# Optimization experiments

Measured on AMD Instinct MI355X. Metric: run time of the kernel, lower is better.

## Reference

```python
import jax, jax.numpy as jnp
import numpy as np

NS, NP, EJ, ER = 10000, 2048, 32768, 32768  # skills, job/resume pairs, edges
D, H = 1536, 8
NEG_SLOPE_ATT = 0.2   # GAT attention leaky_relu
NEG_SLOPE = 0.01      # F.leaky_relu / nn.LeakyReLU default


def setup_inputs() -> dict:
    key = jax.random.key(0)
    ks = jax.random.split(key, 20)
    rn = lambda k, shp, s=1.0: jax.random.normal(k, shp, dtype=jnp.float32) * s
    s_d = 1.0 / np.sqrt(D)
    return {
        "x_skill": rn(ks[0], (NS, D)),
        "x_job": rn(ks[1], (NP, D)),
        "x_resume": rn(ks[2], (NP, D)),
        # GraphConv params (lin_rel has bias, lin_root bias=False in PyG)
        "W_rel": rn(ks[3], (D, D), s_d),
        "b_rel": jnp.zeros((D,), jnp.float32),
        "W_root": rn(ks[4], (D, D), s_d),
        # GATConv params (heads=8, concat=False)
        "W_gat_src": rn(ks[5], (D, H * D), s_d),
        "W_gat_dst": rn(ks[6], (D, H * D), s_d),
        "att_src": rn(ks[7], (H, D), s_d),
        "att_dst": rn(ks[8], (H, D), s_d),
        "b_gat": jnp.zeros((D,), jnp.float32),
        # MLP: [3072 -> 512 -> 128 -> 1]
        "W1": rn(ks[9], (2 * D, 512), 1.0 / np.sqrt(2 * D)),
        "b1": jnp.zeros((512,), jnp.float32),
        "W2": rn(ks[10], (512, 128), 1.0 / np.sqrt(512)),
        "b2": jnp.zeros((128,), jnp.float32),
        "W3": rn(ks[11], (128, 1), 1.0 / np.sqrt(128)),
        "b3": jnp.zeros((1,), jnp.float32),
        # edge lists (src = skill idx, dst = job/resume idx)
        "edge_src_job": jax.random.randint(ks[12], (EJ,), 0, NS, dtype=jnp.int32),
        "edge_dst_job": jax.random.randint(ks[13], (EJ,), 0, NP, dtype=jnp.int32),
        "edge_src_res": jax.random.randint(ks[14], (ER,), 0, NS, dtype=jnp.int32),
        "edge_dst_res": jax.random.randint(ks[15], (ER,), 0, NP, dtype=jnp.int32),
    }


def reference(x_skill, x_job, x_resume, W_rel, b_rel, W_root,
              W_gat_src, W_gat_dst, att_src, att_dst, b_gat,
              W1, b1, W2, b2, W3, b3,
              edge_src_job, edge_dst_job, edge_src_res, edge_dst_res):
    n_pair = x_job.shape[0]

    # --- GraphConv (skill -> job): sum-aggregate then linear + root ---
    agg = jax.ops.segment_sum(x_skill[edge_src_job], edge_dst_job,
                              num_segments=n_pair)                  # [NP, D]
    h_job = agg @ W_rel + b_rel + x_job @ W_root                     # [NP, D]

    # --- GATConv (skill -> resume), heads=H, concat=False, no self-loops ---
    xs = (x_skill @ W_gat_src).reshape(-1, H, D)                     # [NS, H, D]
    xd = (x_resume @ W_gat_dst).reshape(-1, H, D)                    # [NP, H, D]
    a_src = jnp.einsum('nhd,hd->nh', xs, att_src)                    # [NS, H]
    a_dst = jnp.einsum('nhd,hd->nh', xd, att_dst)                    # [NP, H]
    e = jax.nn.leaky_relu(a_src[edge_src_res] + a_dst[edge_dst_res],
                          NEG_SLOPE_ATT)                             # [E, H]
    # segment softmax over edges grouped by destination resume node
    e_max = jax.ops.segment_max(e, edge_dst_res, num_segments=n_pair)
    e_exp = jnp.exp(e - e_max[edge_dst_res])
    denom = jax.ops.segment_sum(e_exp, edge_dst_res, num_segments=n_pair)
    alpha = e_exp / (denom[edge_dst_res] + 1e-16)                    # [E, H]
    msg = xs[edge_src_res] * alpha[:, :, None]                       # [E, H, D]
    out = jax.ops.segment_sum(msg, edge_dst_res, num_segments=n_pair)  # [NP, H, D]
    h_res = out.mean(axis=1) + b_gat                                 # concat=False -> head mean

    # --- combine + MLP ---
    h = jnp.concatenate([jax.nn.leaky_relu(h_job, NEG_SLOPE),
                         jax.nn.leaky_relu(h_res, NEG_SLOPE)], axis=1)  # [NP, 2D]
    h = jax.nn.leaky_relu(h @ W1 + b1, NEG_SLOPE)
    h = jax.nn.leaky_relu(h @ W2 + b2, NEG_SLOPE)
    score = (h @ W3 + b3).squeeze(-1)                                # [NP]
    return score, alpha
```

## Files before the change

### kernel.cpp

```cpp
#include <hip/hip_runtime.h>

#define D_ 1536
#define H_ 8

typedef __attribute__((ext_vector_type(8))) short bf16x8;
typedef __attribute__((ext_vector_type(4))) float f32x4;

__device__ __forceinline__ unsigned short f2bf(float f) {
    unsigned u = __builtin_bit_cast(unsigned, f);
    unsigned r = (u + 0x7fffu + ((u >> 16) & 1u)) >> 16;
    return (unsigned short)r;
}

__device__ __forceinline__ unsigned pack2bf(float a, float b) {
    return (unsigned)f2bf(a) | ((unsigned)f2bf(b) << 16);
}

__device__ __forceinline__ float bflo(unsigned u) { return __builtin_bit_cast(float, u << 16); }
__device__ __forceinline__ float bfhi(unsigned u) { return __builtin_bit_cast(float, u & 0xffff0000u); }

__device__ __forceinline__ void gload16(const void* g, void* l) {
    __builtin_amdgcn_global_load_lds((const __attribute__((address_space(1))) void*)g,
                                     (__attribute__((address_space(3))) void*)l, 16, 0, 0);
}

__global__ __launch_bounds__(256) void k_vmat2(const float* __restrict__ Wsrc,
                                               const float* __restrict__ Wdst,
                                               const float* __restrict__ att_s,
                                               const float* __restrict__ att_d,
                                               float* __restrict__ Vsrc,
                                               float* __restrict__ Vdst) {
    int id = blockIdx.x;
    int sel = id >= D_;
    int d = sel ? id - D_ : id;
    const float4* wr = (const float4*)((sel ? Wdst : Wsrc) + (size_t)d * (H_ * D_));
    const float* at = sel ? att_d : att_s;
    int t = threadIdx.x;
    float part[H_];
    #pragma unroll
    for (int h = 0; h < H_; h++) {
        const float4* ar = (const float4*)(at + h * D_);
        float4 w0 = wr[h * 384 + t];
        float4 a0 = ar[t];
        float s = w0.x * a0.x + w0.y * a0.y + w0.z * a0.z + w0.w * a0.w;
        if (t < 128) {
            float4 w1 = wr[h * 384 + 256 + t];
            float4 a1 = ar[256 + t];
            s += w1.x * a1.x + w1.y * a1.y + w1.z * a1.z + w1.w * a1.w;
        }
        part[h] = s;
    }
    __shared__ float red[4][H_];
    int lane = t & 63, w = t >> 6;
    #pragma unroll
    for (int h = 0; h < H_; h++) {
        float v = part[h];
        for (int o = 32; o; o >>= 1) v += __shfl_down(v, o);
        if (lane == 0) red[w][h] = v;
    }
    __syncthreads();
    if (t < H_) (sel ? Vdst : Vsrc)[d * H_ + t] = red[0][t] + red[1][t] + red[2][t] + red[3][t];
}

__global__ __launch_bounds__(256) void k_a_xsb(const float* __restrict__ x,
                                               const float* __restrict__ V,
                                               float* __restrict__ out,
                                               unsigned* __restrict__ xb) {
    int n = blockIdx.x;
    float part[H_] = {};
    const float2* xr = (const float2*)x + (size_t)n * 768;
    unsigned* ob = xb + (size_t)n * 768;
    #pragma unroll
    for (int j = 0; j < 3; j++) {
        int e = threadIdx.x + j * 256;
        float2 v = xr[e];
        ob[e] = pack2bf(v.x, v.y);
        const float* vp = V + (size_t)(2 * e) * H_;
        #pragma unroll
        for (int h = 0; h < H_; h++) part[h] += v.x * vp[h] + v.y * vp[h + H_];
    }
    __shared__ float red[4][H_];
    int lane = threadIdx.x & 63, w = threadIdx.x >> 6;
    #pragma unroll
    for (int h = 0; h < H_; h++) {
        float v = part[h];
        for (int o = 32; o; o >>= 1) v += __shfl_down(v, o);
        if (lane == 0) red[w][h] = v;
    }
    __syncthreads();
    if (threadIdx.x < H_)
        out[(size_t)n * H_ + threadIdx.x] =
            red[0][threadIdx.x] + red[1][threadIdx.x] + red[2][threadIdx.x] + red[3][threadIdx.x];
}

__global__ __launch_bounds__(256) void k_a(const float* __restrict__ x,
                                           const float* __restrict__ V,
                                           float* __restrict__ out, int N) {
    int n = blockIdx.x;
    if (n >= N) return;
    float part[H_] = {};
    const float* xr = x + (size_t)n * D_;
    #pragma unroll
    for (int j = 0; j < 6; j++) {
        int d = threadIdx.x + j * 256;
        float xv = xr[d];
        const float* vp = V + d * H_;
        #pragma unroll
        for (int h = 0; h < H_; h++) part[h] += xv * vp[h];
    }
    __shared__ float red[4][H_];
    int lane = threadIdx.x & 63, w = threadIdx.x >> 6;
    #pragma unroll
    for (int h = 0; h < H_; h++) {
        float v = part[h];
        for (int o = 32; o; o >>= 1) v += __shfl_down(v, o);
        if (lane == 0) red[w][h] = v;
    }
    __syncthreads();
    if (threadIdx.x < H_)
        out[(size_t)n * H_ + threadIdx.x] =
            red[0][threadIdx.x] + red[1][threadIdx.x] + red[2][threadIdx.x] + red[3][threadIdx.x];
}

__global__ void k_count(const int* __restrict__ dj, int ej, const int* __restrict__ dr, int er,
                        int* cnt_j, int* cnt_r) {
    int i = blockIdx.x * blockDim.x + threadIdx.x;
    if (i < ej) atomicAdd(&cnt_j[dj[i]], 1);
    else if (i < ej + er) atomicAdd(&cnt_r[dr[i - ej]], 1);
}

__global__ void k_scan(const int* __restrict__ cnt_j, int* off_j,
                       const int* __restrict__ cnt_r, int* off_r, int NP) {
    const int* cnt = blockIdx.x ? cnt_r : cnt_j;
    int* off = blockIdx.x ? off_r : off_j;
    int lane = threadIdx.x;
    int chunk = (NP + 63) / 64;
    int base = lane * chunk;
    int sum = 0;
    for (int i = 0; i < chunk; i++) { int idx = base + i; if (idx < NP) sum += cnt[idx]; }
    int incl = sum;
    for (int o = 1; o < 64; o <<= 1) { int t = __shfl_up(incl, o); if (lane >= o) incl += t; }
    int run = incl - sum;
    for (int i = 0; i < chunk; i++) { int idx = base + i; if (idx < NP) { off[idx] = run; run += cnt[idx]; } }
    if (lane == 63) off[NP] = run;
}

__global__ void k_scatter(const int* __restrict__ dj, int ej, const int* __restrict__ dr, int er,
                          const int* __restrict__ off_j, int* fill_j, int* sid_j,
                          const int* __restrict__ off_r, int* fill_r, int* sid_r) {
    int i = blockIdx.x * blockDim.x + threadIdx.x;
    if (i < ej) {
        int p = dj[i];
        int slot = atomicAdd(&fill_j[p], 1);
        sid_j[off_j[p] + slot] = i;
    } else if (i < ej + er) {
        int e = i - ej;
        int p = dr[e];
        int slot = atomicAdd(&fill_r[p], 1);
        sid_r[off_r[p] + slot] = e;
    }
}

__global__ __launch_bounds__(256) void k_agg(const unsigned* __restrict__ xb, const int* __restrict__ src,
                                             const int* __restrict__ sid, const int* __restrict__ cnt,
                                             const int* __restrict__ off,
                                             const float* __restrict__ x_job,
                                             unsigned* __restrict__ cat_u) {
    int p = blockIdx.x;
    int n = cnt[p], o = off[p];
    float2 acc[3] = {};
    int i = 0;
    for (; i + 2 <= n; i += 2) {
        int e0 = sid[o + i], e1 = sid[o + i + 1];
        const unsigned* r0 = xb + (size_t)src[e0] * 768 + threadIdx.x;
        const unsigned* r1 = xb + (size_t)src[e1] * 768 + threadIdx.x;
        unsigned v0[3], v1[3];
        #pragma unroll
        for (int j = 0; j < 3; j++) { v0[j] = r0[j * 256]; v1[j] = r1[j * 256]; }
        #pragma unroll
        for (int j = 0; j < 3; j++) {
            acc[j].x += bflo(v0[j]) + bflo(v1[j]);
            acc[j].y += bfhi(v0[j]) + bfhi(v1[j]);
        }
    }
    if (i < n) {
        int e0 = sid[o + i];
        const unsigned* r0 = xb + (size_t)src[e0] * 768 + threadIdx.x;
        #pragma unroll
        for (int j = 0; j < 3; j++) { unsigned v = r0[j * 256]; acc[j].x += bflo(v); acc[j].y += bfhi(v); }
    }
    unsigned* orow = cat_u + (size_t)p * 1536 + threadIdx.x;
    #pragma unroll
    for (int j = 0; j < 3; j++) orow[j * 256] = pack2bf(acc[j].x, acc[j].y);
    const float2* xjr = (const float2*)x_job + (size_t)p * 768 + threadIdx.x;
    #pragma unroll
    for (int j = 0; j < 3; j++) { float2 v = xjr[j * 256]; orow[768 + j * 256] = pack2bf(v.x, v.y); }
}

__global__ void k_softmax(const float* __restrict__ a_src, const float* __restrict__ a_dst,
                          const int* __restrict__ src, const int* __restrict__ sid,
                          const int* __restrict__ cnt, const int* __restrict__ off,
                          float* __restrict__ alpha_out) {
    int p = blockIdx.x;
    int n = cnt[p], o = off[p];
    if (n == 0) return;
    int lane = threadIdx.x;
    #pragma unroll 1
    for (int h = 0; h < H_; h++) {
        float ad = a_dst[(size_t)p * H_ + h];
        float m = -3.4e38f;
        for (int i = lane; i < n; i += 64) {
            int e = sid[o + i];
            float v = a_src[(size_t)src[e] * H_ + h] + ad;
            v = v >= 0.f ? v : 0.2f * v;
            m = fmaxf(m, v);
        }
        for (int o2 = 32; o2; o2 >>= 1) m = fmaxf(m, __shfl_xor(m, o2));
        float s = 0.f;
        for (int i = lane; i < n; i += 64) {
            int e = sid[o + i];
            float v = a_src[(size_t)src[e] * H_ + h] + ad;
            v = v >= 0.f ? v : 0.2f * v;
            s += expf(v - m);
        }
        for (int o2 = 32; o2; o2 >>= 1) s += __shfl_xor(s, o2);
        float inv = 1.f / (s + 1e-16f);
        for (int i = lane; i < n; i += 64) {
            int e = sid[o + i];
            float v = a_src[(size_t)src[e] * H_ + h] + ad;
            v = v >= 0.f ? v : 0.2f * v;
            alpha_out[(size_t)e * H_ + h] = expf(v - m) * inv;
        }
    }
}

__global__ __launch_bounds__(256) void k_aggatt(const unsigned* __restrict__ xb,
                                                const float* __restrict__ alpha,
                                                const int* __restrict__ src, const int* __restrict__ sid,
                                                const int* __restrict__ cnt, const int* __restrict__ off,
                                                unsigned* __restrict__ aggatt_u) {
    int p = blockIdx.x;
    int n = cnt[p], o = off[p];
    float2 acc[H_][3] = {};
    int i = 0;
    for (; i + 2 <= n; i += 2) {
        int e0 = sid[o + i], e1 = sid[o + i + 1];
        const unsigned* r0 = xb + (size_t)src[e0] * 768 + threadIdx.x;
        const unsigned* r1 = xb + (size_t)src[e1] * 768 + threadIdx.x;
        unsigned v0[3], v1[3];
        #pragma unroll
        for (int j = 0; j < 3; j++) { v0[j] = r0[j * 256]; v1[j] = r1[j * 256]; }
        const float* a0 = alpha + (size_t)e0 * H_;
        const float* a1 = alpha + (size_t)e1 * H_;
        float f0[3][2], f1[3][2];
        #pragma unroll
        for (int j = 0; j < 3; j++) {
            f0[j][0] = bflo(v0[j]); f0[j][1] = bfhi(v0[j]);
            f1[j][0] = bflo(v1[j]); f1[j][1] = bfhi(v1[j]);
        }
        #pragma unroll
        for (int h = 0; h < H_; h++) {
            float w0 = a0[h], w1 = a1[h];
            #pragma unroll
            for (int j = 0; j < 3; j++) {
                acc[h][j].x += w0 * f0[j][0] + w1 * f1[j][0];
                acc[h][j].y += w0 * f0[j][1] + w1 * f1[j][1];
            }
        }
    }
    if (i < n) {
        int e0 = sid[o + i];
        const unsigned* r0 = xb + (size_t)src[e0] * 768 + threadIdx.x;
        unsigned v0[3];
        #pragma unroll
        for (int j = 0; j < 3; j++) v0[j] = r0[j * 256];
        const float* a0 = alpha + (size_t)e0 * H_;
        #pragma unroll
        for (int h = 0; h < H_; h++) {
            float w0 = a0[h];
            #pragma unroll
            for (int j = 0; j < 3; j++) {
                acc[h][j].x += w0 * bflo(v0[j]);
                acc[h][j].y += w0 * bfhi(v0[j]);
            }
        }
    }
    unsigned* orow = aggatt_u + (size_t)p * (H_ * 768) + threadIdx.x;
    #pragma unroll
    for (int h = 0; h < H_; h++)
        #pragma unroll
        for (int j = 0; j < 3; j++)
            orow[h * 768 + j * 256] = pack2bf(acc[h][j].x, acc[h][j].y);
}

template <int GATB>
__global__ __launch_bounds__(256) void k_tr(const float* __restrict__ in, int ldin,
                                            unsigned short* __restrict__ out, int ldout) {
    __shared__ float t[64][65];
    int k0 = blockIdx.y * 64, n0 = blockIdx.x * 64;
    int tx = threadIdx.x & 63, ty = threadIdx.x >> 6;
    #pragma unroll
    for (int i = 0; i < 16; i++) {
        int k = k0 + ty + i * 4;
        const float* rp;
        if (GATB) {
            int d2 = k % D_, h = k / D_;
            rp = in + (size_t)d2 * (H_ * D_) + (size_t)h * D_;
        } else {
            rp = in + (size_t)k * ldin;
        }
        t[ty + i * 4][tx] = rp[n0 + tx];
    }
    __syncthreads();
    int tx2 = threadIdx.x & 31, ty2 = threadIdx.x >> 5;
    #pragma unroll
    for (int i = 0; i < 8; i++) {
        int nl = ty2 + i * 8;
        unsigned v = pack2bf(t[tx2 * 2][nl], t[tx2 * 2 + 1][nl]);
        *(unsigned*)(out + (size_t)(n0 + nl) * ldout + k0 + tx2 * 2) = v;
    }
}

__global__ __launch_bounds__(512, 4) void gemm_sk(const unsigned short* __restrict__ A, int lda,
                                                  const unsigned short* __restrict__ BT, int ldb,
                                                  float* __restrict__ P, int N, int bs, int extra) {
    __shared__ unsigned short As[3][256 * 32];
    __shared__ unsigned short Bs[3][128 * 32];
    int tid = threadIdx.x;
    int lane = tid & 63, wid = tid >> 6;

    int nwg = gridDim.x * gridDim.y;
    int bidh = blockIdx.y * gridDim.x + blockIdx.x;
    int swz = (bidh & 7) * (nwg >> 3) + (bidh >> 3);
    int bn = (swz % gridDim.x) * 128;
    int bm = (swz / gridDim.x) * 256;

    int z = blockIdx.z;
    int nt = bs + (z < extra);
    int kb = z * bs + min(z, extra);
    int kbase = kb * 32;

    int wr = wid >> 1, wc = wid & 1;
    int fr = lane & 15, g = lane >> 4;

    int ra0 = tid >> 2, sa0 = tid & 3;
    int ra1 = (tid + 512) >> 2;
    int sg_a0 = sa0 ^ ((ra0 >> 1) & 3);
    int sg_a1 = sa0 ^ ((ra1 >> 1) & 3);
    int sg_b = sg_a0;

    f32x4 acc[4][4] = {};

    auto stage = [&](int buf, int k0) {
        gload16(A + (size_t)(bm + ra0) * lda + k0 + sg_a0 * 8, &As[buf][tid * 8]);
        gload16(A + (size_t)(bm + ra1) * lda + k0 + sg_a1 * 8, &As[buf][(tid + 512) * 8]);
        gload16(BT + (size_t)(bn + ra0) * ldb + k0 + sg_b * 8, &Bs[buf][tid * 8]);
    };

    stage(0, kbase);
    if (nt > 1) stage(1, kbase + 32);
    for (int t = 0; t < nt; t++) {
        if (t + 2 < nt) {
            stage((t + 2) % 3, kbase + (t + 2) * 32);
            asm volatile("s_waitcnt vmcnt(6)" ::: "memory");
        } else if (t + 1 < nt) {
            asm volatile("s_waitcnt vmcnt(3)" ::: "memory");
        } else {
            asm volatile("s_waitcnt vmcnt(0)" ::: "memory");
        }
        __builtin_amdgcn_s_barrier();
        __builtin_amdgcn_sched_barrier(0);
        int cur = t % 3;
        bf16x8 a[4], b[4];
        #pragma unroll
        for (int mi = 0; mi < 4; mi++) {
            int row = wr * 64 + mi * 16 + fr;
            a[mi] = *(const bf16x8*)(&As[cur][row * 32 + ((g ^ ((row >> 1) & 3)) * 8)]);
        }
        #pragma unroll
        for (int ni = 0; ni < 4; ni++) {
            int row = wc * 64 + ni * 16 + fr;
            b[ni] = *(const bf16x8*)(&Bs[cur][row * 32 + ((g ^ ((row >> 1) & 3)) * 8)]);
        }
        __builtin_amdgcn_s_setprio(1);
        #pragma unroll
        for (int mi = 0; mi < 4; mi++)
            #pragma unroll
            for (int ni = 0; ni < 4; ni++)
                acc[mi][ni] = __builtin_amdgcn_mfma_f32_16x16x32_bf16(a[mi], b[ni], acc[mi][ni], 0, 0, 0);
        __builtin_amdgcn_s_setprio(0);
        __builtin_amdgcn_s_barrier();
        __builtin_amdgcn_sched_barrier(0);
    }

    size_t MN = (size_t)N * (size_t)(gridDim.y * 256);
    float* Pz = P + (size_t)z * MN;
    #pragma unroll
    for (int mi = 0; mi < 4; mi++) {
        int r0 = bm + wr * 64 + mi * 16 + (lane >> 4) * 4;
        #pragma unroll
        for (int ni = 0; ni < 4; ni++) {
            int c = bn + wc * 64 + ni * 16 + (lane & 15);
            #pragma unroll
            for (int j = 0; j < 4; j++)
                Pz[(size_t)(r0 + j) * N + c] = acc[mi][ni][j];
        }
    }
}

template <int OUT_BF16>
__global__ __launch_bounds__(256) void k_reduce(const float* __restrict__ P, int S, int MN, int N,
                                                void* __restrict__ Cout, int ldc,
                                                const float* __restrict__ bias, float scale,
                                                int useLeaky) {
    int idx = (blockIdx.x * 256 + threadIdx.x) * 4;
    if (idx >= MN) return;
    float4 v = *(const float4*)(P + idx);
    for (int s = 1; s < S; s++) {
        float4 t = *(const float4*)(P + (size_t)s * MN + idx);
        v.x += t.x; v.y += t.y; v.z += t.z; v.w += t.w;
    }
    int m = idx / N, n = idx - m * N;
    float vv[4] = {v.x, v.y, v.z, v.w};
    #pragma unroll
    for (int j = 0; j < 4; j++) {
        float x = vv[j] * scale + bias[n + j];
        if (useLeaky) x = x >= 0.f ? x : 0.01f * x;
        if (OUT_BF16) ((unsigned short*)Cout)[(size_t)m * ldc + n + j] = f2bf(x);
        else ((float*)Cout)[(size_t)m * ldc + n + j] = x;
    }
}

__global__ __launch_bounds__(256) void k_mlp2(const unsigned short* __restrict__ h1b,
                                              const float* __restrict__ W2,
                                              const float* __restrict__ b2,
                                              const float* __restrict__ W3,
                                              const float* __restrict__ b3,
                                              float* __restrict__ score) {
    __shared__ unsigned h1s[8][256];
    __shared__ float red[4][4];
    int p0 = blockIdx.x * 8;
    int tid = threadIdx.x;
    const unsigned* hsrc = (const unsigned*)h1b + (size_t)p0 * 256;
    #pragma unroll
    for (int i = 0; i < 8; i++) {
        int idx = tid + i * 256;
        h1s[idx >> 8][idx & 255] = hsrc[idx];
    }
    __syncthreads();
    int c = tid & 127, rg = tid >> 7;
    float acc[4] = {};
    for (int k = 0; k < 512; k += 2) {
        float w0 = W2[(size_t)k * 128 + c];
        float w1 = W2[(size_t)(k + 1) * 128 + c];
        #pragma unroll
        for (int r = 0; r < 4; r++) {
            unsigned hv = h1s[rg * 4 + r][k >> 1];
            acc[r] += bflo(hv) * w0 + bfhi(hv) * w1;
        }
    }
    float w3 = W3[c];
    float pr[4];
    #pragma unroll
    for (int r = 0; r < 4; r++) {
        float v = acc[r] + b2[c];
        v = v >= 0.f ? v : 0.01f * v;
        pr[r] = v * w3;
    }
    #pragma unroll
    for (int r = 0; r < 4; r++)
        for (int o = 32; o; o >>= 1) pr[r] += __shfl_down(pr[r], o);
    int w = tid >> 6;
    if ((tid & 63) == 0) {
        #pragma unroll
        for (int r = 0; r < 4; r++) red[w][r] = pr[r];
    }
    __syncthreads();
    if (tid < 8) {
        int rg2 = tid >> 2, r = tid & 3;
        float s = red[rg2 * 2][r] + red[rg2 * 2 + 1][r] + b3[0];
        score[p0 + rg2 * 4 + r] = s;
    }
}

extern "C" void kernel_launch(void* const* d_in, const int* in_sizes, int n_in,
                              void* d_out, int out_size, void* d_ws, size_t ws_size,
                              hipStream_t stream) {
    const float* x_skill = (const float*)d_in[0];
    const float* x_job   = (const float*)d_in[1];
    const float* x_resume= (const float*)d_in[2];
    const float* W_rel   = (const float*)d_in[3];
    const float* b_rel   = (const float*)d_in[4];
    const float* W_root  = (const float*)d_in[5];
    const float* W_gs    = (const float*)d_in[6];
    const float* W_gd    = (const float*)d_in[7];
    const float* att_s   = (const float*)d_in[8];
    const float* att_d   = (const float*)d_in[9];
    const float* b_gat   = (const float*)d_in[10];
    const float* W1      = (const float*)d_in[11];
    const float* b1      = (const float*)d_in[12];
    const float* W2      = (const float*)d_in[13];
    const float* b2      = (const float*)d_in[14];
    const float* W3      = (const float*)d_in[15];
    const float* b3      = (const float*)d_in[16];
    const int* esj = (const int*)d_in[17];
    const int* edj = (const int*)d_in[18];
    const int* esr = (const int*)d_in[19];
    const int* edr = (const int*)d_in[20];

    const int NS = in_sizes[0] / D_;
    const int NP = in_sizes[1] / D_;
    const int EJ = in_sizes[17];
    const int ER = in_sizes[19];

    float* score = (float*)d_out;
    float* alpha = score + NP;

    char* ws = (char*)d_ws;
    size_t off = 0;
    auto alloc = [&](size_t bytes) -> void* {
        void* p = ws + off;
        off = (off + bytes + 255) & ~(size_t)255;
        return p;
    };

    int* cnt_j  = (int*)alloc((size_t)4 * NP * sizeof(int));
    int* fill_j = cnt_j + NP;
    int* cnt_r  = cnt_j + 2 * NP;
    int* fill_r = cnt_j + 3 * NP;
    int* off_j  = (int*)alloc((size_t)(NP + 1) * sizeof(int));
    int* off_r  = (int*)alloc((size_t)(NP + 1) * sizeof(int));
    int* sid_j  = (int*)alloc((size_t)EJ * sizeof(int));
    int* sid_r  = (int*)alloc((size_t)ER * sizeof(int));
    float* Vsrc = (float*)alloc((size_t)D_ * H_ * 4);
    float* Vdst = (float*)alloc((size_t)D_ * H_ * 4);
    float* a_src= (float*)alloc((size_t)NS * H_ * 4);
    float* a_dst= (float*)alloc((size_t)NP * H_ * 4);
    unsigned short* cat_in = (unsigned short*)alloc((size_t)NP * 2 * D_ * 2);
    unsigned short* aggatt = (unsigned short*)alloc((size_t)NP * H_ * D_ * 2);
    unsigned short* BT1    = (unsigned short*)alloc((size_t)D_ * 2 * D_ * 2);
    unsigned short* BTg    = (unsigned short*)alloc((size_t)D_ * H_ * D_ * 2);
    unsigned short* BTw1   = (unsigned short*)alloc((size_t)512 * 2 * D_ * 2);
    unsigned short* hcat   = (unsigned short*)alloc((size_t)NP * 2 * D_ * 2);
    unsigned short* h1b    = (unsigned short*)alloc((size_t)NP * 512 * 2);
    float* Pbuf = (float*)alloc((size_t)5 * NP * D_ * 4);
    unsigned* xsb = (unsigned*)Pbuf;

    hipMemsetAsync(cnt_j, 0, (size_t)4 * NP * sizeof(int), stream);

    k_tr<0><<<dim3(D_ / 64, D_ / 64), 256, 0, stream>>>(W_rel, D_, BT1, 2 * D_);
    k_tr<0><<<dim3(D_ / 64, D_ / 64), 256, 0, stream>>>(W_root, D_, BT1 + D_, 2 * D_);
    k_tr<1><<<dim3(D_ / 64, (H_ * D_) / 64), 256, 0, stream>>>(W_gs, 0, BTg, H_ * D_);
    k_tr<0><<<dim3(512 / 64, (2 * D_) / 64), 256, 0, stream>>>(W1, 512, BTw1, 2 * D_);

    k_vmat2<<<2 * D_, 256, 0, stream>>>(W_gs, W_gd, att_s, att_d, Vsrc, Vdst);
    k_a_xsb<<<NS, 256, 0, stream>>>(x_skill, Vsrc, a_src, xsb);
    k_a<<<NP, 256, 0, stream>>>(x_resume, Vdst, a_dst, NP);

    int egrid = (EJ + ER + 255) / 256;
    k_count<<<egrid, 256, 0, stream>>>(edj, EJ, edr, ER, cnt_j, cnt_r);
    k_scan<<<2, 64, 0, stream>>>(cnt_j, off_j, cnt_r, off_r, NP);
    k_scatter<<<egrid, 256, 0, stream>>>(edj, EJ, edr, ER, off_j, fill_j, sid_j, off_r, fill_r, sid_r);

    k_agg<<<NP, 256, 0, stream>>>(xsb, esj, sid_j, cnt_j, off_j, x_job, (unsigned*)cat_in);
    k_softmax<<<NP, 64, 0, stream>>>(a_src, a_dst, esr, sid_r, cnt_r, off_r, alpha);
    k_aggatt<<<NP, 256, 0, stream>>>(xsb, alpha, esr, sid_r, cnt_r, off_r, (unsigned*)aggatt);

    const int MN_f = NP * D_;
    const int MN_1 = NP * 512;

    gemm_sk<<<dim3(D_ / 128, NP / 256, 5), 512, 0, stream>>>(
        cat_in, 2 * D_, BT1, 2 * D_, Pbuf, D_, 19, 1);
    k_reduce<1><<<MN_f / 1024, 256, 0, stream>>>(Pbuf, 5, MN_f, D_, hcat, 2 * D_, b_rel, 1.f, 1);

    gemm_sk<<<dim3(D_ / 128, NP / 256, 5), 512, 0, stream>>>(
        aggatt, H_ * D_, BTg, H_ * D_, Pbuf, D_, 76, 4);
    k_reduce<1><<<MN_f / 1024, 256, 0, stream>>>(Pbuf, 5, MN_f, D_, hcat + D_, 2 * D_, b_gat, 1.f / H_, 1);

    gemm_sk<<<dim3(512 / 128, NP / 256, 8), 512, 0, stream>>>(
        hcat, 2 * D_, BTw1, 2 * D_, Pbuf, 512, 12, 0);
    k_reduce<1><<<MN_1 / 1024, 256, 0, stream>>>(Pbuf, 8, MN_1, 512, h1b, 512, b1, 1.f, 1);

    k_mlp2<<<NP / 8, 256, 0, stream>>>(h1b, W2, b2, W3, b3, score);
}
```

Baseline: 449.0 us.

## Fuse Vsrc into transpose, merge attention-score kernels, split aggregation columns, retune split-K

Computes the source attention projection inside the GAT weight transpose using atomics, so W_gat_src is no longer read a second time by k_vmat2. Merges the skill and resume attention-score kernels into one launch. Splits the edge aggregation kernels across three column blocks to raise parallelism and lower register pressure. Adds a single-wave fast path in the softmax for nodes with at most 64 edges, which does all heads in one pass with vector loads. Changes the split-K factors of the three GEMMs to 6, 6 and 16, which needs a larger partial buffer.

```diff
diff --git a/kernel.cpp b/kernel.cpp
--- a/kernel.cpp
+++ b/kernel.cpp
@@ -24,22 +24,16 @@
                                      (__attribute__((address_space(3))) void*)l, 16, 0, 0);
 }
 
-__global__ __launch_bounds__(256) void k_vmat2(const float* __restrict__ Wsrc,
-                                               const float* __restrict__ Wdst,
-                                               const float* __restrict__ att_s,
+__global__ __launch_bounds__(256) void k_vmat2(const float* __restrict__ Wdst,
                                                const float* __restrict__ att_d,
-                                               float* __restrict__ Vsrc,
                                                float* __restrict__ Vdst) {
-    int id = blockIdx.x;
-    int sel = id >= D_;
-    int d = sel ? id - D_ : id;
-    const float4* wr = (const float4*)((sel ? Wdst : Wsrc) + (size_t)d * (H_ * D_));
-    const float* at = sel ? att_d : att_s;
+    int d = blockIdx.x;
+    const float4* wr = (const float4*)(Wdst + (size_t)d * (H_ * D_));
     int t = threadIdx.x;
     float part[H_];
     #pragma unroll
     for (int h = 0; h < H_; h++) {
-        const float4* ar = (const float4*)(at + h * D_);
+        const float4* ar = (const float4*)(att_d + h * D_);
         float4 w0 = wr[h * 384 + t];
         float4 a0 = ar[t];
         float s = w0.x * a0.x + w0.y * a0.y + w0.z * a0.z + w0.w * a0.w;
@@ -59,22 +53,29 @@
         if (lane == 0) red[w][h] = v;
     }
     __syncthreads();
-    if (t < H_) (sel ? Vdst : Vsrc)[d * H_ + t] = red[0][t] + red[1][t] + red[2][t] + red[3][t];
-}
-
-__global__ __launch_bounds__(256) void k_a_xsb(const float* __restrict__ x,
-                                               const float* __restrict__ V,
-                                               float* __restrict__ out,
-                                               unsigned* __restrict__ xb) {
+    if (t < H_) Vdst[d * H_ + t] = red[0][t] + red[1][t] + red[2][t] + red[3][t];
+}
+
+__global__ __launch_bounds__(256) void k_a2(const float* __restrict__ xs,
+                                            const float* __restrict__ xr,
+                                            const float* __restrict__ Vs,
+                                            const float* __restrict__ Vd,
+                                            float* __restrict__ a_s,
+                                            float* __restrict__ a_d,
+                                            unsigned* __restrict__ xb, int NS) {
     int n = blockIdx.x;
+    int skill = n < NS;
+    int row = skill ? n : n - NS;
+    const float2* xrow = (const float2*)(skill ? xs : xr) + (size_t)row * 768;
+    const float* V = skill ? Vs : Vd;
+    float* out = (skill ? a_s : a_d) + (size_t)row * H_;
+    unsigned* ob = xb + (size_t)row * 768;
     float part[H_] = {};
-    const float2* xr = (const float2*)x + (size_t)n * 768;
-    unsigned* ob = xb + (size_t)n * 768;
     #pragma unroll
     for (int j = 0; j < 3; j++) {
         int e = threadIdx.x + j * 256;
-        float2 v = xr[e];
-        ob[e] = pack2bf(v.x, v.y);
+        float2 v = xrow[e];
+        if (skill) ob[e] = pack2bf(v.x, v.y);
         const float* vp = V + (size_t)(2 * e) * H_;
         #pragma unroll
         for (int h = 0; h < H_; h++) part[h] += v.x * vp[h] + v.y * vp[h + H_];
@@ -88,38 +89,8 @@
         if (lane == 0) red[w][h] = v;
     }
     __syncthreads();
-    if (threadIdx.x < H_)
-        out[(size_t)n * H_ + threadIdx.x] =
-            red[0][threadIdx.x] + red[1][threadIdx.x] + red[2][threadIdx.x] + red[3][threadIdx.x];
-}
-
-__global__ __launch_bounds__(256) void k_a(const float* __restrict__ x,
-                                           const float* __restrict__ V,
-                                           float* __restrict__ out, int N) {
-    int n = blockIdx.x;
-    if (n >= N) return;
-    float part[H_] = {};
-    const float* xr = x + (size_t)n * D_;
-    #pragma unroll
-    for (int j = 0; j < 6; j++) {
-        int d = threadIdx.x + j * 256;
-        float xv = xr[d];
-        const float* vp = V + d * H_;
-        #pragma unroll
-        for (int h = 0; h < H_; h++) part[h] += xv * vp[h];
-    }
-    __shared__ float red[4][H_];
-    int lane = threadIdx.x & 63, w = threadIdx.x >> 6;
-    #pragma unroll
-    for (int h = 0; h < H_; h++) {
-        float v = part[h];
-        for (int o = 32; o; o >>= 1) v += __shfl_down(v, o);
-        if (lane == 0) red[w][h] = v;
-    }
-    __syncthreads();
-    if (threadIdx.x < H_)
-        out[(size_t)n * H_ + threadIdx.x] =
-            red[0][threadIdx.x] + red[1][threadIdx.x] + red[2][threadIdx.x] + red[3][threadIdx.x];
+    if (threadIdx.x < H_) out[threadIdx.x] =
+        red[0][threadIdx.x] + red[1][threadIdx.x] + red[2][threadIdx.x] + red[3][threadIdx.x];
 }
 
 __global__ void k_count(const int* __restrict__ dj, int ej, const int* __restrict__ dr, int er,
@@ -166,35 +137,26 @@
                                              const int* __restrict__ off,
                                              const float* __restrict__ x_job,
                                              unsigned* __restrict__ cat_u) {
-    int p = blockIdx.x;
+    int p = blockIdx.x, j = blockIdx.y;
     int n = cnt[p], o = off[p];
-    float2 acc[3] = {};
+    int col = j * 256 + threadIdx.x;
+    float2 acc = {0.f, 0.f};
     int i = 0;
     for (; i + 2 <= n; i += 2) {
         int e0 = sid[o + i], e1 = sid[o + i + 1];
-        const unsigned* r0 = xb + (size_t)src[e0] * 768 + threadIdx.x;
-        const unsigned* r1 = xb + (size_t)src[e1] * 768 + threadIdx.x;
-        unsigned v0[3], v1[3];
-        #pragma unroll
-        for (int j = 0; j < 3; j++) { v0[j] = r0[j * 256]; v1[j] = r1[j * 256]; }
-        #pragma unroll
-        for (int j = 0; j < 3; j++) {
-            acc[j].x += bflo(v0[j]) + bflo(v1[j]);
-            acc[j].y += bfhi(v0[j]) + bfhi(v1[j]);
-        }
+        unsigned v0 = xb[(size_t)src[e0] * 768 + col];
+        unsigned v1 = xb[(size_t)src[e1] * 768 + col];
+        acc.x += bflo(v0) + bflo(v1);
+        acc.y += bfhi(v0) + bfhi(v1);
     }
     if (i < n) {
-        int e0 = sid[o + i];
-        const unsigned* r0 = xb + (size_t)src[e0] * 768 + threadIdx.x;
-        #pragma unroll
-        for (int j = 0; j < 3; j++) { unsigned v = r0[j * 256]; acc[j].x += bflo(v); acc[j].y += bfhi(v); }
-    }
-    unsigned* orow = cat_u + (size_t)p * 1536 + threadIdx.x;
-    #pragma unroll
-    for (int j = 0; j < 3; j++) orow[j * 256] = pack2bf(acc[j].x, acc[j].y);
-    const float2* xjr = (const float2*)x_job + (size_t)p * 768 + threadIdx.x;
-    #pragma unroll
-    for (int j = 0; j < 3; j++) { float2 v = xjr[j * 256]; orow[768 + j * 256] = pack2bf(v.x, v.y); }
+        unsigned v = xb[(size_t)src[sid[o + i]] * 768 + col];
+        acc.x += bflo(v); acc.y += bfhi(v);
+    }
+    unsigned* orow = cat_u + (size_t)p * 1536;
+    orow[col] = pack2bf(acc.x, acc.y);
+    float2 vj = ((const float2*)x_job)[(size_t)p * 768 + col];
+    orow[768 + col] = pack2bf(vj.x, vj.y);
 }
 
 __global__ void k_softmax(const float* __restrict__ a_src, const float* __restrict__ a_dst,
@@ -205,31 +167,68 @@
     int n = cnt[p], o = off[p];
     if (n == 0) return;
     int lane = threadIdx.x;
-    #pragma unroll 1
-    for (int h = 0; h < H_; h++) {
-        float ad = a_dst[(size_t)p * H_ + h];
-        float m = -3.4e38f;
-        for (int i = lane; i < n; i += 64) {
-            int e = sid[o + i];
-            float v = a_src[(size_t)src[e] * H_ + h] + ad;
-            v = v >= 0.f ? v : 0.2f * v;
-            m = fmaxf(m, v);
-        }
-        for (int o2 = 32; o2; o2 >>= 1) m = fmaxf(m, __shfl_xor(m, o2));
-        float s = 0.f;
-        for (int i = lane; i < n; i += 64) {
-            int e = sid[o + i];
-            float v = a_src[(size_t)src[e] * H_ + h] + ad;
-            v = v >= 0.f ? v : 0.2f * v;
-            s += expf(v - m);
-        }
-        for (int o2 = 32; o2; o2 >>= 1) s += __shfl_xor(s, o2);
-        float inv = 1.f / (s + 1e-16f);
-        for (int i = lane; i < n; i += 64) {
-            int e = sid[o + i];
-            float v = a_src[(size_t)src[e] * H_ + h] + ad;
-            v = v >= 0.f ? v : 0.2f * v;
-            alpha_out[(size_t)e * H_ + h] = expf(v - m) * inv;
+    float4 ad0 = *(const float4*)(a_dst + (size_t)p * H_);
+    float4 ad1 = *(const float4*)(a_dst + (size_t)p * H_ + 4);
+    float adv[8] = {ad0.x, ad0.y, ad0.z, ad0.w, ad1.x, ad1.y, ad1.z, ad1.w};
+    if (n <= 64) {
+        int e = 0;
+        float v[8];
+        if (lane < n) {
+            e = sid[o + lane];
+            int s = src[e];
+            float4 s0 = *(const float4*)(a_src + (size_t)s * H_);
+            float4 s1 = *(const float4*)(a_src + (size_t)s * H_ + 4);
+            float sv[8] = {s0.x, s0.y, s0.z, s0.w, s1.x, s1.y, s1.z, s1.w};
+            #pragma unroll
+            for (int h = 0; h < H_; h++) {
+                float t = sv[h] + adv[h];
+                v[h] = t >= 0.f ? t : 0.2f * t;
+            }
+        } else {
+            #pragma unroll
+            for (int h = 0; h < H_; h++) v[h] = -3.4e38f;
+        }
+        float ex[8];
+        #pragma unroll
+        for (int h = 0; h < H_; h++) {
+            float m = v[h];
+            for (int o2 = 32; o2; o2 >>= 1) m = fmaxf(m, __shfl_xor(m, o2));
+            float ev = (lane < n) ? expf(v[h] - m) : 0.f;
+            float s = ev;
+            for (int o2 = 32; o2; o2 >>= 1) s += __shfl_xor(s, o2);
+            ex[h] = ev / (s + 1e-16f);
+        }
+        if (lane < n) {
+            *(float4*)(alpha_out + (size_t)e * H_) = make_float4(ex[0], ex[1], ex[2], ex[3]);
+            *(float4*)(alpha_out + (size_t)e * H_ + 4) = make_float4(ex[4], ex[5], ex[6], ex[7]);
+        }
+    } else {
+        #pragma unroll 1
+        for (int h = 0; h < H_; h++) {
+            float ad = adv[h];
+            float m = -3.4e38f;
+            for (int i = lane; i < n; i += 64) {
+                int e = sid[o + i];
+                float v = a_src[(size_t)src[e] * H_ + h] + ad;
+                v = v >= 0.f ? v : 0.2f * v;
+                m = fmaxf(m, v);
+            }
+            for (int o2 = 32; o2; o2 >>= 1) m = fmaxf(m, __shfl_xor(m, o2));
+            float s = 0.f;
+            for (int i = lane; i < n; i += 64) {
+                int e = sid[o + i];
+                float v = a_src[(size_t)src[e] * H_ + h] + ad;
+                v = v >= 0.f ? v : 0.2f * v;
+                s += expf(v - m);
+            }
+            for (int o2 = 32; o2; o2 >>= 1) s += __shfl_xor(s, o2);
+            float inv = 1.f / (s + 1e-16f);
+            for (int i = lane; i < n; i += 64) {
+                int e = sid[o + i];
+                float v = a_src[(size_t)src[e] * H_ + h] + ad;
+                v = v >= 0.f ? v : 0.2f * v;
+                alpha_out[(size_t)e * H_ + h] = expf(v - m) * inv;
+            }
         }
     }
 }
@@ -239,63 +238,43 @@
                                                 const int* __restrict__ src, const int* __restrict__ sid,
                                                 const int* __restrict__ cnt, const int* __restrict__ off,
                                                 unsigned* __restrict__ aggatt_u) {
-    int p = blockIdx.x;
+    int p = blockIdx.x, j = blockIdx.y;
     int n = cnt[p], o = off[p];
-    float2 acc[H_][3] = {};
+    int col = j * 256 + threadIdx.x;
+    float2 acc[H_] = {};
     int i = 0;
     for (; i + 2 <= n; i += 2) {
         int e0 = sid[o + i], e1 = sid[o + i + 1];
-        const unsigned* r0 = xb + (size_t)src[e0] * 768 + threadIdx.x;
-        const unsigned* r1 = xb + (size_t)src[e1] * 768 + threadIdx.x;
-        unsigned v0[3], v1[3];
-        #pragma unroll
-        for (int j = 0; j < 3; j++) { v0[j] = r0[j * 256]; v1[j] = r1[j * 256]; }
+        unsigned v0 = xb[(size_t)src[e0] * 768 + col];
+        unsigned v1 = xb[(size_t)src[e1] * 768 + col];
+        float l0 = bflo(v0), h0 = bfhi(v0), l1 = bflo(v1), h1 = bfhi(v1);
         const float* a0 = alpha + (size_t)e0 * H_;
         const float* a1 = alpha + (size_t)e1 * H_;
-        float f0[3][2], f1[3][2];
-        #pragma unroll
-        for (int j = 0; j < 3; j++) {
-            f0[j][0] = bflo(v0[j]); f0[j][1] = bfhi(v0[j]);
-            f1[j][0] = bflo(v1[j]); f1[j][1] = bfhi(v1[j]);
-        }
         #pragma unroll
         for (int h = 0; h < H_; h++) {
             float w0 = a0[h], w1 = a1[h];
-            #pragma unroll
-            for (int j = 0; j < 3; j++) {
-                acc[h][j].x += w0 * f0[j][0] + w1 * f1[j][0];
-                acc[h][j].y += w0 * f0[j][1] + w1 * f1[j][1];
-            }
+            acc[h].x += w0 * l0 + w1 * l1;
+            acc[h].y += w0 * h0 + w1 * h1;
         }
     }
     if (i < n) {
         int e0 = sid[o + i];
-        const unsigned* r0 = xb + (size_t)src[e0] * 768 + threadIdx.x;
-        unsigned v0[3];
-        #pragma unroll
-        for (int j = 0; j < 3; j++) v0[j] = r0[j * 256];
+        unsigned v0 = xb[(size_t)src[e0] * 768 + col];
+        float l0 = bflo(v0), h0 = bfhi(v0);
         const float* a0 = alpha + (size_t)e0 * H_;
         #pragma unroll
-        for (int h = 0; h < H_; h++) {
-            float w0 = a0[h];
-            #pragma unroll
-            for (int j = 0; j < 3; j++) {
-                acc[h][j].x += w0 * bflo(v0[j]);
-                acc[h][j].y += w0 * bfhi(v0[j]);
-            }
-        }
-    }
-    unsigned* orow = aggatt_u + (size_t)p * (H_ * 768) + threadIdx.x;
+        for (int h = 0; h < H_; h++) { acc[h].x += a0[h] * l0; acc[h].y += a0[h] * h0; }
+    }
+    unsigned* orow = aggatt_u + (size_t)p * (H_ * 768);
     #pragma unroll
     for (int h = 0; h < H_; h++)
-        #pragma unroll
-        for (int j = 0; j < 3; j++)
-            orow[h * 768 + j * 256] = pack2bf(acc[h][j].x, acc[h][j].y);
+        orow[h * 768 + col] = pack2bf(acc[h].x, acc[h].y);
 }
 
 template <int GATB>
 __global__ __launch_bounds__(256) void k_tr(const float* __restrict__ in, int ldin,
-                                            unsigned short* __restrict__ out, int ldout) {
+                                            unsigned short* __restrict__ out, int ldout,
+                                            const float* __restrict__ att, float* __restrict__ V) {
     __shared__ float t[64][65];
     int k0 = blockIdx.y * 64, n0 = blockIdx.x * 64;
     int tx = threadIdx.x & 63, ty = threadIdx.x >> 6;
@@ -318,6 +297,17 @@
         int nl = ty2 + i * 8;
         unsigned v = pack2bf(t[tx2 * 2][nl], t[tx2 * 2 + 1][nl]);
         *(unsigned*)(out + (size_t)(n0 + nl) * ldout + k0 + tx2 * 2) = v;
+    }
+    if (GATB) {
+        int h = k0 / D_, d2b = k0 - h * D_;
+        int kl = threadIdx.x >> 2, q = threadIdx.x & 3;
+        const float* ar = att + (size_t)h * D_ + n0 + q * 16;
+        float s = 0.f;
+        #pragma unroll
+        for (int i = 0; i < 16; i++) s += t[kl][q * 16 + i] * ar[i];
+        s += __shfl_xor(s, 1);
+        s += __shfl_xor(s, 2);
+        if (q == 0) atomicAdd(&V[(size_t)(d2b + kl) * H_ + h], s);
     }
 }
 
@@ -543,43 +533,43 @@
     unsigned short* BTw1   = (unsigned short*)alloc((size_t)512 * 2 * D_ * 2);
     unsigned short* hcat   = (unsigned short*)alloc((size_t)NP * 2 * D_ * 2);
     unsigned short* h1b    = (unsigned short*)alloc((size_t)NP * 512 * 2);
-    float* Pbuf = (float*)alloc((size_t)5 * NP * D_ * 4);
+    float* Pbuf = (float*)alloc((size_t)6 * NP * D_ * 4);
     unsigned* xsb = (unsigned*)Pbuf;
 
     hipMemsetAsync(cnt_j, 0, (size_t)4 * NP * sizeof(int), stream);
-
-    k_tr<0><<<dim3(D_ / 64, D_ / 64), 256, 0, stream>>>(W_rel, D_, BT1, 2 * D_);
-    k_tr<0><<<dim3(D_ / 64, D_ / 64), 256, 0, stream>>>(W_root, D_, BT1 + D_, 2 * D_);
-    k_tr<1><<<dim3(D_ / 64, (H_ * D_) / 64), 256, 0, stream>>>(W_gs, 0, BTg, H_ * D_);
-    k_tr<0><<<dim3(512 / 64, (2 * D_) / 64), 256, 0, stream>>>(W1, 512, BTw1, 2 * D_);
-
-    k_vmat2<<<2 * D_, 256, 0, stream>>>(W_gs, W_gd, att_s, att_d, Vsrc, Vdst);
-    k_a_xsb<<<NS, 256, 0, stream>>>(x_skill, Vsrc, a_src, xsb);
-    k_a<<<NP, 256, 0, stream>>>(x_resume, Vdst, a_dst, NP);
+    hipMemsetAsync(Vsrc, 0, (size_t)D_ * H_ * sizeof(float), stream);
+
+    k_tr<0><<<dim3(D_ / 64, D_ / 64), 256, 0, stream>>>(W_rel, D_, BT1, 2 * D_, nullptr, nullptr);
+    k_tr<0><<<dim3(D_ / 64, D_ / 64), 256, 0, stream>>>(W_root, D_, BT1 + D_, 2 * D_, nullptr, nullptr);
+    k_tr<1><<<dim3(D_ / 64, (H_ * D_) / 64), 256, 0, stream>>>(W_gs, 0, BTg, H_ * D_, att_s, Vsrc);
+    k_tr<0><<<dim3(512 / 64, (2 * D_) / 64), 256, 0, stream>>>(W1, 512, BTw1, 2 * D_, nullptr, nullptr);
+
+    k_vmat2<<<D_, 256, 0, stream>>>(W_gd, att_d, Vdst);
+    k_a2<<<NS + NP, 256, 0, stream>>>(x_skill, x_resume, Vsrc, Vdst, a_src, a_dst, xsb, NS);
 
     int egrid = (EJ + ER + 255) / 256;
     k_count<<<egrid, 256, 0, stream>>>(edj, EJ, edr, ER, cnt_j, cnt_r);
     k_scan<<<2, 64, 0, stream>>>(cnt_j, off_j, cnt_r, off_r, NP);
     k_scatter<<<egrid, 256, 0, stream>>>(edj, EJ, edr, ER, off_j, fill_j, sid_j, off_r, fill_r, sid_r);
 
-    k_agg<<<NP, 256, 0, stream>>>(xsb, esj, sid_j, cnt_j, off_j, x_job, (unsigned*)cat_in);
+    k_agg<<<dim3(NP, 3), 256, 0, stream>>>(xsb, esj, sid_j, cnt_j, off_j, x_job, (unsigned*)cat_in);
     k_softmax<<<NP, 64, 0, stream>>>(a_src, a_dst, esr, sid_r, cnt_r, off_r, alpha);
-    k_aggatt<<<NP, 256, 0, stream>>>(xsb, alpha, esr, sid_r, cnt_r, off_r, (unsigned*)aggatt);
+    k_aggatt<<<dim3(NP, 3), 256, 0, stream>>>(xsb, alpha, esr, sid_r, cnt_r, off_r, (unsigned*)aggatt);
 
     const int MN_f = NP * D_;
     const int MN_1 = NP * 512;
 
-    gemm_sk<<<dim3(D_ / 128, NP / 256, 5), 512, 0, stream>>>(
-        cat_in, 2 * D_, BT1, 2 * D_, Pbuf, D_, 19, 1);
-    k_reduce<1><<<MN_f / 1024, 256, 0, stream>>>(Pbuf, 5, MN_f, D_, hcat, 2 * D_, b_rel, 1.f, 1);
-
-    gemm_sk<<<dim3(D_ / 128, NP / 256, 5), 512, 0, stream>>>(
-        aggatt, H_ * D_, BTg, H_ * D_, Pbuf, D_, 76, 4);
-    k_reduce<1><<<MN_f / 1024, 256, 0, stream>>>(Pbuf, 5, MN_f, D_, hcat + D_, 2 * D_, b_gat, 1.f / H_, 1);
-
-    gemm_sk<<<dim3(512 / 128, NP / 256, 8), 512, 0, stream>>>(
-        hcat, 2 * D_, BTw1, 2 * D_, Pbuf, 512, 12, 0);
-    k_reduce<1><<<MN_1 / 1024, 256, 0, stream>>>(Pbuf, 8, MN_1, 512, h1b, 512, b1, 1.f, 1);
+    gemm_sk<<<dim3(D_ / 128, NP / 256, 6), 512, 0, stream>>>(
+        cat_in, 2 * D_, BT1, 2 * D_, Pbuf, D_, 16, 0);
+    k_reduce<1><<<MN_f / 1024, 256, 0, stream>>>(Pbuf, 6, MN_f, D_, hcat, 2 * D_, b_rel, 1.f, 1);
+
+    gemm_sk<<<dim3(D_ / 128, NP / 256, 6), 512, 0, stream>>>(
+        aggatt, H_ * D_, BTg, H_ * D_, Pbuf, D_, 64, 0);
+    k_reduce<1><<<MN_f / 1024, 256, 0, stream>>>(Pbuf, 6, MN_f, D_, hcat + D_, 2 * D_, b_gat, 1.f / H_, 1);
+
+    gemm_sk<<<dim3(512 / 128, NP / 256, 16), 512, 0, stream>>>(
+        hcat, 2 * D_, BTw1, 2 * D_, Pbuf, 512, 6, 0);
+    k_reduce<1><<<MN_1 / 1024, 256, 0, stream>>>(Pbuf, 16, MN_1, 512, h1b, 512, b1, 1.f, 1);
 
     k_mlp2<<<NP / 8, 256, 0, stream>>>(h1b, W2, b2, W3, b3, score);
 }
```

After: 470.1 us. 1.05x slower.
